# Optimization experiments

Measured on AMD Instinct MI355X. Metric: run time of the kernel, lower is better.

## Reference

```python
import jax, jax.numpy as jnp
import numpy as np

B, T, D, H = 4, 4096, 1024, 16
HD = D // H
K = 3  # local_kernel
DIL = 1
EPS = 1e-5


def _ln(x, g, b):
    m = x.mean(-1, keepdims=True)
    v = ((x - m) ** 2).mean(-1, keepdims=True)
    return (x - m) * jax.lax.rsqrt(v + EPS) * g + b


def setup_inputs() -> dict:
    key = jax.random.key(0)
    ks = jax.random.split(key, 6)
    s = 0.02
    return {
        "x": jax.random.normal(ks[0], (B, T, D), jnp.float32),
        "ln_g": jnp.ones((D,), jnp.float32),
        "ln_b": jnp.zeros((D,), jnp.float32),
        "w_qkv": (jax.random.normal(ks[1], (3 * D, D), jnp.float32) * s),  # torch Linear weight [out,in]
        "conv_w": (jax.random.normal(ks[2], (D, 1, K), jnp.float32) * s),  # depthwise conv [D,1,K]
        "conv_b": jnp.zeros((D,), jnp.float32),
        "gln_g": jnp.ones((D,), jnp.float32),
        "gln_b": jnp.zeros((D,), jnp.float32),
        "w_gate": (jax.random.normal(ks[3], (D, D), jnp.float32) * s),
        "b_gate": jnp.zeros((D,), jnp.float32),
        "w_out": (jax.random.normal(ks[4], (D, D), jnp.float32) * s),
        "b_out": jnp.zeros((D,), jnp.float32),
    }


def reference(x, ln_g, ln_b, w_qkv, conv_w, conv_b, gln_g, gln_b, w_gate, b_gate, w_out, b_out):
    b, t, d = x.shape
    x_norm = _ln(x, ln_g, ln_b)

    # QKV projection (no bias)
    qkv = x_norm @ w_qkv.T  # [b,t,3d]
    q, k, v = jnp.split(qkv, 3, axis=-1)
    to_heads = lambda z: z.reshape(b, t, H, HD).transpose(0, 2, 1, 3)  # [b,h,t,hd]
    q, k, v = to_heads(q), to_heads(k), to_heads(v)

    # ELU-feature linear attention (no denominator, matching source)
    phi_q = jax.nn.elu(q) + 1.0
    phi_k = jax.nn.elu(k) + 1.0
    kv = jnp.einsum('bhtd,bhte->bhde', phi_k, v)      # [b,h,hd,hd]
    y_att = jnp.einsum('bhtd,bhde->bhte', phi_q, kv)  # [b,h,t,hd]
    y_att = y_att.transpose(0, 2, 1, 3).reshape(b, t, d)

    # Depthwise local conv branch on x_norm
    pad = (K - 1) // 2 * DIL
    y_local = jax.lax.conv_general_dilated(
        x_norm.transpose(0, 2, 1), conv_w,
        window_strides=(1,), padding=[(pad, pad)], rhs_dilation=(DIL,),
        feature_group_count=d, dimension_numbers=('NCH', 'OIH', 'NCH'))
    y_local = (y_local + conv_b[None, :, None]).transpose(0, 2, 1)  # [b,t,d]

    # Gate: LN -> Linear -> Sigmoid on raw x
    g = jax.nn.sigmoid(_ln(x, gln_g, gln_b) @ w_gate.T + b_gate)

    y = g * y_att + (1.0 - g) * y_local
    return x + (y @ w_out.T + b_out)
```

## Files before the change

kernel.cpp:

```cpp
#include <hip/hip_runtime.h>
#include <hip/hip_bf16.h>

#define B_ 4
#define T_ 4096
#define D_ 1024
#define H_ 16
#define M_ (B_*T_)
#define KV_CHUNKS 16

typedef short bf16x8 __attribute__((ext_vector_type(8)));
typedef float f32x4 __attribute__((ext_vector_type(4)));

__device__ __forceinline__ float b2f(unsigned short h){
  union { unsigned u; float f; } x; x.u = ((unsigned)h) << 16; return x.f;
}
__device__ __forceinline__ unsigned short f2b(float f){
  union { float f; unsigned u; } x; x.f = f;
  unsigned r = x.u + 0x7FFFu + ((x.u >> 16) & 1u);
  return (unsigned short)(r >> 16);
}

__device__ __forceinline__ void ld_lds16(const unsigned short* g, unsigned short* l){
  __builtin_amdgcn_global_load_lds(
      (const __attribute__((address_space(1))) unsigned int*)(unsigned long long)g,
      (__attribute__((address_space(3))) unsigned int*)(unsigned int)(unsigned long long)l,
      16, 0, 0);
}

__global__ __launch_bounds__(256) void f32_to_bf16(const float* __restrict__ src,
                                                   unsigned short* __restrict__ dst, int n){
  int i = (blockIdx.x*256 + threadIdx.x)*4;
  if (i < n){
    float4 v = *(const float4*)(src + i);
    ushort4 o; o.x=f2b(v.x); o.y=f2b(v.y); o.z=f2b(v.z); o.w=f2b(v.w);
    *(ushort4*)(dst + i) = o;
  }
}

__global__ __launch_bounds__(256) void ln_dual(
    const float* __restrict__ x,
    const float* __restrict__ g1, const float* __restrict__ b1,
    const float* __restrict__ g2, const float* __restrict__ b2,
    unsigned short* __restrict__ xn, unsigned short* __restrict__ xg){
  int row = blockIdx.x;
  int tid = threadIdx.x;
  const float4* xr = (const float4*)(x + (size_t)row*D_);
  float4 v = xr[tid];
  float s  = v.x+v.y+v.z+v.w;
  float ss = v.x*v.x + v.y*v.y + v.z*v.z + v.w*v.w;
  #pragma unroll
  for (int o=32;o>0;o>>=1){ s += __shfl_down(s,o,64); ss += __shfl_down(ss,o,64); }
  __shared__ float red[8];
  int lane = tid & 63, wv = tid >> 6;
  if (lane==0){ red[wv]=s; red[4+wv]=ss; }
  __syncthreads();
  s  = red[0]+red[1]+red[2]+red[3];
  ss = red[4]+red[5]+red[6]+red[7];
  float mean = s * (1.f/D_);
  float var  = ss*(1.f/D_) - mean*mean;
  float inv  = rsqrtf(var + 1e-5f);
  int c = tid*4;
  float4 ga = *(const float4*)(g1+c), ba = *(const float4*)(b1+c);
  float4 gb = *(const float4*)(g2+c), bb = *(const float4*)(b2+c);
  float nx=(v.x-mean)*inv, ny=(v.y-mean)*inv, nz=(v.z-mean)*inv, nw=(v.w-mean)*inv;
  size_t base = (size_t)row*D_ + c;
  ushort4 o1, o2;
  o1.x=f2b(nx*ga.x+ba.x); o1.y=f2b(ny*ga.y+ba.y); o1.z=f2b(nz*ga.z+ba.z); o1.w=f2b(nw*ga.w+ba.w);
  o2.x=f2b(nx*gb.x+bb.x); o2.y=f2b(ny*gb.y+bb.y); o2.z=f2b(nz*gb.z+bb.z); o2.w=f2b(nw*gb.w+bb.w);
  *(ushort4*)(xn+base) = o1;
  *(ushort4*)(xg+base) = o2;
}

template<int EPI>
__global__ __launch_bounds__(256, 3) void gemm_bt(
    const unsigned short* __restrict__ A, const unsigned short* __restrict__ Bw,
    int N, int K,
    const float* __restrict__ bias, const float* __restrict__ resid,
    unsigned short* __restrict__ Cb, float* __restrict__ Cf){
  __shared__ unsigned short sA[128*32];
  __shared__ unsigned short sB[128*32];
  int tid = threadIdx.x;
  int lane = tid & 63, wv = tid >> 6;
  int m0 = blockIdx.x * 128, n0 = blockIdx.y * 128;
  int srow = wv*32 + (lane>>2);
  int scol = (((lane&3) ^ ((lane>>3)&3)))*8;
  const unsigned short* gA = A + (size_t)(m0+srow)*K + scol;
  const unsigned short* gB = Bw + (size_t)(n0+srow)*K + scol;
  unsigned short* lA = sA + wv*1024;
  unsigned short* lB = sB + wv*1024;
  f32x4 zero = {0.f,0.f,0.f,0.f};
  f32x4 acc[4][4];
  #pragma unroll
  for (int i=0;i<4;i++){ acc[i][0]=zero; acc[i][1]=zero; acc[i][2]=zero; acc[i][3]=zero; }
  int wm = wv & 1, wn = wv >> 1;
  int fr = lane & 15;
  int fk = ((lane >> 4) * 8) ^ (((fr>>1)&3)<<3);
  for (int kk = 0; kk < K; kk += 32){
    __syncthreads();
    ld_lds16(gA,              lA);
    ld_lds16(gA + (size_t)16*K, lA + 512);
    ld_lds16(gB,              lB);
    ld_lds16(gB + (size_t)16*K, lB + 512);
    gA += 32; gB += 32;
    __syncthreads();
    bf16x8 af[4], bfr[4];
    #pragma unroll
    for (int i=0;i<4;i++) af[i]  = *(const bf16x8*)(sA + (wm*64 + i*16 + fr)*32 + fk);
    #pragma unroll
    for (int j=0;j<4;j++) bfr[j] = *(const bf16x8*)(sB + (wn*64 + j*16 + fr)*32 + fk);
    #pragma unroll
    for (int i=0;i<4;i++)
      #pragma unroll
      for (int j=0;j<4;j++)
        acc[i][j] = __builtin_amdgcn_mfma_f32_16x16x32_bf16(af[i], bfr[j], acc[i][j], 0,0,0);
  }
  int er = (lane>>4)*4;
  int ec = lane & 15;
  #pragma unroll
  for (int i=0;i<4;i++){
    #pragma unroll
    for (int r=0;r<4;r++){
      int m = m0 + wm*64 + i*16 + er + r;
      size_t rowoff = (size_t)m * N;
      #pragma unroll
      for (int j=0;j<4;j++){
        int n = n0 + wn*64 + j*16 + ec;
        float v = acc[i][j][r];
        if (EPI == 0){
          Cb[rowoff + n] = f2b(v);
        } else if (EPI == 1){
          v += bias[n];
          v = 1.f/(1.f + __expf(-v));
          Cb[rowoff + n] = f2b(v);
        } else {
          v += bias[n] + resid[rowoff + n];
          Cf[rowoff + n] = v;
        }
      }
    }
  }
}

__global__ __launch_bounds__(256) void kv_partial(const unsigned short* __restrict__ qkv,
                                                  float* __restrict__ part){
  int bh = blockIdx.x, chunk = blockIdx.y;
  int b = bh >> 4, h = bh & 15;
  int tid = threadIdx.x;
  int d = tid & 63, wv = tid >> 6;
  __shared__ float sk[512], sv[512];
  float acc[16];
  #pragma unroll
  for (int j=0;j<16;j++) acc[j] = 0.f;
  size_t base = ((size_t)(b*T_) + (size_t)chunk*(T_/KV_CHUNKS)) * 3072 + h*64;
  for (int ts=0; ts<(T_/KV_CHUNKS); ts+=8){
    __syncthreads();
    int li = tid & 127;
    int tt = li >> 4;
    int e  = (li & 15) * 4;
    size_t off = base + (size_t)(ts+tt)*3072 + e;
    if (tid < 128){
      ushort4 kr = *(const ushort4*)(qkv + off + 1024);
      float k0=b2f(kr.x), k1=b2f(kr.y), k2=b2f(kr.z), k3=b2f(kr.w);
      float4 ph;
      ph.x = k0>0.f ? k0+1.f : __expf(k0);
      ph.y = k1>0.f ? k1+1.f : __expf(k1);
      ph.z = k2>0.f ? k2+1.f : __expf(k2);
      ph.w = k3>0.f ? k3+1.f : __expf(k3);
      *(float4*)(sk + tt*64 + e) = ph;
    } else {
      ushort4 vr = *(const ushort4*)(qkv + off + 2048);
      float4 vv; vv.x=b2f(vr.x); vv.y=b2f(vr.y); vv.z=b2f(vr.z); vv.w=b2f(vr.w);
      *(float4*)(sv + tt*64 + e) = vv;
    }
    __syncthreads();
    #pragma unroll
    for (int t8=0;t8<8;t8++){
      float pk = sk[t8*64 + d];
      const float4* v4 = (const float4*)(sv + t8*64 + wv*16);
      float4 a0=v4[0], a1=v4[1], a2=v4[2], a3=v4[3];
      acc[0] +=pk*a0.x; acc[1] +=pk*a0.y; acc[2] +=pk*a0.z; acc[3] +=pk*a0.w;
      acc[4] +=pk*a1.x; acc[5] +=pk*a1.y; acc[6] +=pk*a1.z; acc[7] +=pk*a1.w;
      acc[8] +=pk*a2.x; acc[9] +=pk*a2.y; acc[10]+=pk*a2.z; acc[11]+=pk*a2.w;
      acc[12]+=pk*a3.x; acc[13]+=pk*a3.y; acc[14]+=pk*a3.w==0?pk*a3.z:pk*a3.z; acc[15]+=pk*a3.w;
    }
  }
  float* pp = part + (((size_t)chunk*64 + bh)*4096) + d*64 + wv*16;
  #pragma unroll
  for (int j=0;j<16;j++) pp[j] = acc[j];
}

__global__ __launch_bounds__(256) void kv_reduce(const float* __restrict__ part,
                                                 unsigned short* __restrict__ kvb){
  int i = blockIdx.x*256 + threadIdx.x;
  float s = 0.f;
  #pragma unroll
  for (int c=0;c<KV_CHUNKS;c++) s += part[(size_t)c*262144 + i];
  int bh = i >> 12, de = i & 4095;
  int d = de >> 6, e = de & 63;
  kvb[(bh<<12) + e*64 + d] = f2b(s);
}

__global__ __launch_bounds__(256) void attn_mfma(
    const unsigned short* __restrict__ qkv, const unsigned short* __restrict__ kvb,
    const unsigned short* __restrict__ xn, const unsigned short* __restrict__ gsig,
    const float* __restrict__ conv_w, const float* __restrict__ conv_b,
    unsigned short* __restrict__ y){
  int bh = blockIdx.x;
  int b = bh >> 4, h = bh & 15;
  int t0 = blockIdx.y * 128;
  int tid = threadIdx.x, lane = tid & 63, wv = tid >> 6;
  __shared__ __align__(16) char smem[128*68*4];
  unsigned short* sA = (unsigned short*)smem;
  unsigned short* sB = sA + 128*72;
  float* sC = (float*)smem;
  __shared__ float sW[64*4];
  if (tid < 64){
    int d = h*64 + tid;
    sW[tid*4+0] = conv_w[d*3];
    sW[tid*4+1] = conv_w[d*3+1];
    sW[tid*4+2] = conv_w[d*3+2];
    sW[tid*4+3] = conv_b[d];
  }
  #pragma unroll
  for (int it=0; it<4; it++){
    int idx = it*256 + tid;
    int r = idx >> 3, c = (idx & 7)*8;
    size_t gaddr = ((size_t)(b*T_ + t0 + r))*3072 + h*64 + c;
    bf16x8 u = *(const bf16x8*)(qkv + gaddr);
    bf16x8 o;
    #pragma unroll
    for (int q=0;q<8;q++){
      float f = b2f((unsigned short)u[q]);
      f = f > 0.f ? f + 1.f : __expf(f);
      o[q] = (short)f2b(f);
    }
    *(bf16x8*)(sA + r*72 + c) = o;
  }
  #pragma unroll
  for (int it=0; it<2; it++){
    int idx = it*256 + tid;
    int r = idx >> 3, c = (idx & 7)*8;
    *(bf16x8*)(sB + r*72 + c) = *(const bf16x8*)(kvb + ((size_t)bh<<12) + r*64 + c);
  }
  __syncthreads();
  int fr = lane & 15, fk = (lane >> 4)*8;
  bf16x8 af[2][2], bfr[4][2];
  #pragma unroll
  for (int i=0;i<2;i++)
    #pragma unroll
    for (int ks=0;ks<2;ks++)
      af[i][ks] = *(const bf16x8*)(sA + (wv*32 + i*16 + fr)*72 + ks*32 + fk);
  #pragma unroll
  for (int j=0;j<4;j++)
    #pragma unroll
    for (int ks=0;ks<2;ks++)
      bfr[j][ks] = *(const bf16x8*)(sB + (j*16 + fr)*72 + ks*32 + fk);
  __syncthreads();
  f32x4 zero = {0.f,0.f,0.f,0.f};
  f32x4 acc[2][4];
  #pragma unroll
  for (int i=0;i<2;i++){ acc[i][0]=zero; acc[i][1]=zero; acc[i][2]=zero; acc[i][3]=zero; }
  #pragma unroll
  for (int ks=0;ks<2;ks++)
    #pragma unroll
    for (int i=0;i<2;i++)
      #pragma unroll
      for (int j=0;j<4;j++)
        acc[i][j] = __builtin_amdgcn_mfma_f32_16x16x32_bf16(af[i][ks], bfr[j][ks], acc[i][j], 0,0,0);
  int er = (lane>>4)*4, ec = lane & 15;
  #pragma unroll
  for (int i=0;i<2;i++)
    #pragma unroll
    for (int j=0;j<4;j++)
      #pragma unroll
      for (int r=0;r<4;r++)
        sC[(wv*32 + i*16 + er + r)*68 + j*16 + ec] = acc[i][j][r];
  __syncthreads();
  int row = tid >> 1, cb0 = (tid & 1)*32;
  int t = t0 + row;
  size_t gb = ((size_t)(b*T_ + t))*1024 + h*64 + cb0;
  #pragma unroll
  for (int c8=0; c8<4; c8++){
    int cc = cb0 + c8*8;
    const float4* cp = (const float4*)(sC + row*68 + cc);
    float4 cv0 = cp[0], cv1 = cp[1];
    bf16x8 gv = *(const bf16x8*)(gsig + gb + c8*8);
    bf16x8 xc = *(const bf16x8*)(xn + gb + c8*8);
    bf16x8 xm = {0,0,0,0,0,0,0,0}, xp = {0,0,0,0,0,0,0,0};
    if (t > 0)     xm = *(const bf16x8*)(xn + gb + c8*8 - 1024);
    if (t < T_-1)  xp = *(const bf16x8*)(xn + gb + c8*8 + 1024);
    bf16x8 o;
    #pragma unroll
    for (int q=0;q<8;q++){
      const float* w = sW + (cc + q)*4;
      float yl = b2f((unsigned short)xm[q])*w[0] + b2f((unsigned short)xc[q])*w[1]
               + b2f((unsigned short)xp[q])*w[2] + w[3];
      float ya = (q < 4) ? ((const float*)&cv0)[q] : ((const float*)&cv1)[q-4];
      float gg = b2f((unsigned short)gv[q]);
      o[q] = (short)f2b(gg*ya + (1.f-gg)*yl);
    }
    *(bf16x8*)(y + gb + c8*8) = o;
  }
}

extern "C" void kernel_launch(void* const* d_in, const int* in_sizes, int n_in,
                              void* d_out, int out_size, void* d_ws, size_t ws_size,
                              hipStream_t stream){
  const float* x      = (const float*)d_in[0];
  const float* ln_g   = (const float*)d_in[1];
  const float* ln_b   = (const float*)d_in[2];
  const float* w_qkv  = (const float*)d_in[3];
  const float* conv_w = (const float*)d_in[4];
  const float* conv_b = (const float*)d_in[5];
  const float* gln_g  = (const float*)d_in[6];
  const float* gln_b  = (const float*)d_in[7];
  const float* w_gate = (const float*)d_in[8];
  const float* b_gate = (const float*)d_in[9];
  const float* w_out  = (const float*)d_in[10];
  const float* b_out  = (const float*)d_in[11];
  float* out = (float*)d_out;

  char* ws = (char*)d_ws;
  size_t off = 0;
  auto alloc = [&](size_t bytes){ void* p = ws + off; off += (bytes + 255) & ~(size_t)255; return p; };
  unsigned short* wqkv_b  = (unsigned short*)alloc((size_t)3072*1024*2);
  unsigned short* wgate_b = (unsigned short*)alloc((size_t)1024*1024*2);
  unsigned short* wout_b  = (unsigned short*)alloc((size_t)1024*1024*2);
  unsigned short* xn      = (unsigned short*)alloc((size_t)M_*D_*2);
  unsigned short* xg      = (unsigned short*)alloc((size_t)M_*D_*2);
  unsigned short* qkv     = (unsigned short*)alloc((size_t)M_*3072*2);
  unsigned short* gy      = (unsigned short*)alloc((size_t)M_*D_*2);
  float* part             = (float*)alloc((size_t)KV_CHUNKS*64*4096*4);
  unsigned short* kvb     = (unsigned short*)alloc((size_t)64*4096*2);

  f32_to_bf16<<<3072*1024/1024, 256, 0, stream>>>(w_qkv,  wqkv_b,  3072*1024);
  f32_to_bf16<<<1024*1024/1024, 256, 0, stream>>>(w_gate, wgate_b, 1024*1024);
  f32_to_bf16<<<1024*1024/1024, 256, 0, stream>>>(w_out,  wout_b,  1024*1024);

  ln_dual<<<M_, 256, 0, stream>>>(x, ln_g, ln_b, gln_g, gln_b, xn, xg);

  gemm_bt<0><<<dim3(128,24), 256, 0, stream>>>(xn, wqkv_b, 3072, 1024, nullptr, nullptr, qkv, nullptr);

  kv_partial<<<dim3(64,KV_CHUNKS), 256, 0, stream>>>(qkv, part);
  kv_reduce<<<1024, 256, 0, stream>>>(part, kvb);

  gemm_bt<1><<<dim3(128,8), 256, 0, stream>>>(xg, wgate_b, 1024, 1024, b_gate, nullptr, gy, nullptr);

  attn_mfma<<<dim3(64,32), 256, 0, stream>>>(qkv, kvb, xn, gy, conv_w, conv_b, gy);

  gemm_bt<2><<<dim3(128,8), 256, 0, stream>>>(gy, wout_b, 1024, 1024, b_out, x, nullptr, out);
}
```

Before: 473.8 us.

## Fuse QKV and gate GEMMs, merge weight conversions, smaller-tile output GEMM

Concatenates the QKV and gate weights so a single GEMM launch computes both projections, picking its A input and epilogue per block column. The three weight-conversion launches become one, and the output projection switches to a 64x128 tile kernel so it launches twice as many blocks. The aim is to cut launch overhead and tail under-utilisation on the smaller 1024-wide GEMMs. Branching on blockIdx inside the fused GEMM adds a little divergence-free overhead, and the smaller tiles reuse each loaded B tile across fewer rows.

```diff
diff --git a/kernel.cpp b/kernel.cpp
--- a/kernel.cpp
+++ b/kernel.cpp
@@ -27,14 +27,18 @@
       16, 0, 0);
 }
 
-__global__ __launch_bounds__(256) void f32_to_bf16(const float* __restrict__ src,
-                                                   unsigned short* __restrict__ dst, int n){
+__global__ __launch_bounds__(256) void conv_all(
+    const float* __restrict__ w_qkv, const float* __restrict__ w_gate,
+    const float* __restrict__ w_out,
+    unsigned short* __restrict__ wcomb, unsigned short* __restrict__ woutb){
   int i = (blockIdx.x*256 + threadIdx.x)*4;
-  if (i < n){
-    float4 v = *(const float4*)(src + i);
-    ushort4 o; o.x=f2b(v.x); o.y=f2b(v.y); o.z=f2b(v.z); o.w=f2b(v.w);
-    *(ushort4*)(dst + i) = o;
-  }
+  const float* src; unsigned short* dst; int off;
+  if (i < 3145728){ src = w_qkv; dst = wcomb; off = i; }
+  else if (i < 4194304){ src = w_gate; dst = wcomb + 3145728; off = i - 3145728; }
+  else { src = w_out; dst = woutb; off = i - 4194304; }
+  float4 v = *(const float4*)(src + off);
+  ushort4 o; o.x=f2b(v.x); o.y=f2b(v.y); o.z=f2b(v.z); o.w=f2b(v.w);
+  *(ushort4*)(dst + off) = o;
 }
 
 __global__ __launch_bounds__(256) void ln_dual(
@@ -71,20 +75,22 @@
   *(ushort4*)(xg+base) = o2;
 }
 
-template<int EPI>
-__global__ __launch_bounds__(256, 3) void gemm_bt(
-    const unsigned short* __restrict__ A, const unsigned short* __restrict__ Bw,
-    int N, int K,
-    const float* __restrict__ bias, const float* __restrict__ resid,
-    unsigned short* __restrict__ Cb, float* __restrict__ Cf){
+__global__ __launch_bounds__(256, 3) void gemm_fused(
+    const unsigned short* __restrict__ xn, const unsigned short* __restrict__ xg,
+    const unsigned short* __restrict__ Bw,
+    const float* __restrict__ b_gate,
+    unsigned short* __restrict__ qkv, unsigned short* __restrict__ gy){
   __shared__ unsigned short sA[128*32];
   __shared__ unsigned short sB[128*32];
+  const int K = 1024;
   int tid = threadIdx.x;
   int lane = tid & 63, wv = tid >> 6;
   int m0 = blockIdx.x * 128, n0 = blockIdx.y * 128;
+  bool isGate = (blockIdx.y >= 24);
+  const unsigned short* A = isGate ? xg : xn;
   int srow = wv*32 + (lane>>2);
   int scol = (((lane&3) ^ ((lane>>3)&3)))*8;
-  const unsigned short* gA = A + (size_t)(m0+srow)*K + scol;
+  const unsigned short* gA = A  + (size_t)(m0+srow)*K + scol;
   const unsigned short* gB = Bw + (size_t)(n0+srow)*K + scol;
   unsigned short* lA = sA + wv*1024;
   unsigned short* lB = sB + wv*1024;
@@ -97,9 +103,9 @@
   int fk = ((lane >> 4) * 8) ^ (((fr>>1)&3)<<3);
   for (int kk = 0; kk < K; kk += 32){
     __syncthreads();
-    ld_lds16(gA,              lA);
+    ld_lds16(gA,                lA);
     ld_lds16(gA + (size_t)16*K, lA + 512);
-    ld_lds16(gB,              lB);
+    ld_lds16(gB,                lB);
     ld_lds16(gB + (size_t)16*K, lB + 512);
     gA += 32; gB += 32;
     __syncthreads();
@@ -121,21 +127,77 @@
     #pragma unroll
     for (int r=0;r<4;r++){
       int m = m0 + wm*64 + i*16 + er + r;
-      size_t rowoff = (size_t)m * N;
       #pragma unroll
       for (int j=0;j<4;j++){
         int n = n0 + wn*64 + j*16 + ec;
         float v = acc[i][j][r];
-        if (EPI == 0){
-          Cb[rowoff + n] = f2b(v);
-        } else if (EPI == 1){
-          v += bias[n];
+        if (!isGate){
+          qkv[(size_t)m*3072 + n] = f2b(v);
+        } else {
+          int nl = n - 3072;
+          v += b_gate[nl];
           v = 1.f/(1.f + __expf(-v));
-          Cb[rowoff + n] = f2b(v);
-        } else {
-          v += bias[n] + resid[rowoff + n];
-          Cf[rowoff + n] = v;
+          gy[(size_t)m*1024 + nl] = f2b(v);
         }
+      }
+    }
+  }
+}
+
+__global__ __launch_bounds__(256, 4) void gemm64_out(
+    const unsigned short* __restrict__ A, const unsigned short* __restrict__ Bw,
+    const float* __restrict__ bias, const float* __restrict__ resid,
+    float* __restrict__ Cf){
+  __shared__ unsigned short sA[64*32];
+  __shared__ unsigned short sB[128*32];
+  const int K = 1024, N = 1024;
+  int tid = threadIdx.x;
+  int lane = tid & 63, wv = tid >> 6;
+  int m0 = blockIdx.x * 64, n0 = blockIdx.y * 128;
+  int srowA = wv*16 + (lane>>2);
+  int srowB = wv*32 + (lane>>2);
+  int scol = (((lane&3) ^ ((lane>>3)&3)))*8;
+  const unsigned short* gA = A  + (size_t)(m0+srowA)*K + scol;
+  const unsigned short* gB = Bw + (size_t)(n0+srowB)*K + scol;
+  unsigned short* lA = sA + wv*512;
+  unsigned short* lB = sB + wv*1024;
+  f32x4 zero = {0.f,0.f,0.f,0.f};
+  f32x4 acc[2][4];
+  #pragma unroll
+  for (int i=0;i<2;i++){ acc[i][0]=zero; acc[i][1]=zero; acc[i][2]=zero; acc[i][3]=zero; }
+  int wm = wv & 1, wn = wv >> 1;
+  int fr = lane & 15;
+  int fk = ((lane >> 4) * 8) ^ (((fr>>1)&3)<<3);
+  for (int kk = 0; kk < K; kk += 32){
+    __syncthreads();
+    ld_lds16(gA,                lA);
+    ld_lds16(gB,                lB);
+    ld_lds16(gB + (size_t)16*K, lB + 512);
+    gA += 32; gB += 32;
+    __syncthreads();
+    bf16x8 af[2], bfr[4];
+    #pragma unroll
+    for (int i=0;i<2;i++) af[i]  = *(const bf16x8*)(sA + (wm*32 + i*16 + fr)*32 + fk);
+    #pragma unroll
+    for (int j=0;j<4;j++) bfr[j] = *(const bf16x8*)(sB + (wn*64 + j*16 + fr)*32 + fk);
+    #pragma unroll
+    for (int i=0;i<2;i++)
+      #pragma unroll
+      for (int j=0;j<4;j++)
+        acc[i][j] = __builtin_amdgcn_mfma_f32_16x16x32_bf16(af[i], bfr[j], acc[i][j], 0,0,0);
+  }
+  int er = (lane>>4)*4;
+  int ec = lane & 15;
+  #pragma unroll
+  for (int i=0;i<2;i++){
+    #pragma unroll
+    for (int r=0;r<4;r++){
+      int m = m0 + wm*32 + i*16 + er + r;
+      size_t rowoff = (size_t)m * N;
+      #pragma unroll
+      for (int j=0;j<4;j++){
+        int n = n0 + wn*64 + j*16 + ec;
+        Cf[rowoff + n] = acc[i][j][r] + bias[n] + resid[rowoff + n];
       }
     }
   }
@@ -181,7 +243,7 @@
       acc[0] +=pk*a0.x; acc[1] +=pk*a0.y; acc[2] +=pk*a0.z; acc[3] +=pk*a0.w;
       acc[4] +=pk*a1.x; acc[5] +=pk*a1.y; acc[6] +=pk*a1.z; acc[7] +=pk*a1.w;
       acc[8] +=pk*a2.x; acc[9] +=pk*a2.y; acc[10]+=pk*a2.z; acc[11]+=pk*a2.w;
-      acc[12]+=pk*a3.x; acc[13]+=pk*a3.y; acc[14]+=pk*a3.w==0?pk*a3.z:pk*a3.z; acc[15]+=pk*a3.w;
+      acc[12]+=pk*a3.x; acc[13]+=pk*a3.y; acc[14]+=pk*a3.z; acc[15]+=pk*a3.w;
     }
   }
   float* pp = part + (((size_t)chunk*64 + bh)*4096) + d*64 + wv*16;
@@ -323,8 +385,7 @@
   char* ws = (char*)d_ws;
   size_t off = 0;
   auto alloc = [&](size_t bytes){ void* p = ws + off; off += (bytes + 255) & ~(size_t)255; return p; };
-  unsigned short* wqkv_b  = (unsigned short*)alloc((size_t)3072*1024*2);
-  unsigned short* wgate_b = (unsigned short*)alloc((size_t)1024*1024*2);
+  unsigned short* wcomb   = (unsigned short*)alloc((size_t)4096*1024*2);
   unsigned short* wout_b  = (unsigned short*)alloc((size_t)1024*1024*2);
   unsigned short* xn      = (unsigned short*)alloc((size_t)M_*D_*2);
   unsigned short* xg      = (unsigned short*)alloc((size_t)M_*D_*2);
@@ -333,20 +394,16 @@
   float* part             = (float*)alloc((size_t)KV_CHUNKS*64*4096*4);
   unsigned short* kvb     = (unsigned short*)alloc((size_t)64*4096*2);
 
-  f32_to_bf16<<<3072*1024/1024, 256, 0, stream>>>(w_qkv,  wqkv_b,  3072*1024);
-  f32_to_bf16<<<1024*1024/1024, 256, 0, stream>>>(w_gate, wgate_b, 1024*1024);
-  f32_to_bf16<<<1024*1024/1024, 256, 0, stream>>>(w_out,  wout_b,  1024*1024);
+  conv_all<<<5120, 256, 0, stream>>>(w_qkv, w_gate, w_out, wcomb, wout_b);
 
   ln_dual<<<M_, 256, 0, stream>>>(x, ln_g, ln_b, gln_g, gln_b, xn, xg);
 
-  gemm_bt<0><<<dim3(128,24), 256, 0, stream>>>(xn, wqkv_b, 3072, 1024, nullptr, nullptr, qkv, nullptr);
+  gemm_fused<<<dim3(128,32), 256, 0, stream>>>(xn, xg, wcomb, b_gate, qkv, gy);
 
   kv_partial<<<dim3(64,KV_CHUNKS), 256, 0, stream>>>(qkv, part);
   kv_reduce<<<1024, 256, 0, stream>>>(part, kvb);
 
-  gemm_bt<1><<<dim3(128,8), 256, 0, stream>>>(xg, wgate_b, 1024, 1024, b_gate, nullptr, gy, nullptr);
-
   attn_mfma<<<dim3(64,32), 256, 0, stream>>>(qkv, kvb, xn, gy, conv_w, conv_b, gy);
 
-  gemm_bt<2><<<dim3(128,8), 256, 0, stream>>>(gy, wout_b, 1024, 1024, b_out, x, nullptr, out);
-}
+  gemm64_out<<<dim3(256,8), 256, 0, stream>>>(gy, wout_b, b_out, x, out);
+}
```

Result: slower. 495.5 us (+4.6%).
